# Performance work log

Hardware: AMD Instinct MI355X
Metric: run time of the kernel (lower is better)

## Reference

```python
import jax, jax.numpy as jnp
import numpy as np

N_GENOMES = 30000
N_GENES = 240000
N_SAMPLES = 128
N_SEQS = 80000


def setup_inputs() -> dict:
    key = jax.random.key(0)
    k0, k1, k2, k3, k4 = jax.random.split(key, 5)
    A = jax.random.normal(k0, (N_GENOMES, N_SAMPLES), dtype=jnp.float32)  # log-abundance
    B = jax.random.normal(k1, (N_GENOMES, N_SAMPLES), dtype=jnp.float32)  # log-PTR
    pos = jax.random.uniform(k2, (N_GENES,), dtype=jnp.float32)           # dist from ori, in [0,1)
    genome_idx = jnp.sort(jax.random.randint(k3, (N_GENES,), 0, N_GENOMES))  # block one-hot of `members`
    seq_idx = jax.random.randint(k4, (N_GENES,), 0, N_SEQS)               # gene -> md5 sequence map
    return {"A": A, "B": B, "pos": pos, "genome_idx": genome_idx, "seq_idx": seq_idx}


def reference(A, B, pos, genome_idx, seq_idx):
    # G = members @ A + 1 - dists @ B, where members/dists are one-hot per gene row
    # -> gather rows of A and B by genome assignment, scale B row by gene position.
    G = A[genome_idx] + 1.0 - pos[:, None] * B[genome_idx]   # (m, s)
    # gene_to_seq @ exp(G) -> segment sum of exp(G) over gene->sequence assignment
    return jax.ops.segment_sum(jnp.exp(G), seq_idx, num_segments=N_SEQS)  # (k, s)
```

## Files before the change

### kernel.cpp

```cpp
#include <hip/hip_runtime.h>
#include <hip/hip_fp16.h>

#define N_GENOMES 30000
#define N_GENES   240000
#define N_SAMPLES 128
#define N_SEQS    80000
#define CAP       32

#define SCATTER_BLOCKS  ((N_GENES + 255) / 256)
#define COMPRESS_BLOCKS ((N_GENOMES * 32) / 256)

typedef float        f32x4 __attribute__((ext_vector_type(4)));
typedef unsigned int u32x4 __attribute__((ext_vector_type(4)));

#define LOG2E 1.4426950408889634f

#if __has_builtin(__builtin_amdgcn_exp2f)
#define EXP2F(x) __builtin_amdgcn_exp2f(x)
#else
#define EXP2F(x) exp2f(x)
#endif

__global__ __launch_bounds__(256) void prep_kernel(
    const float* __restrict__ A,
    const float* __restrict__ B,
    const float* __restrict__ pos,
    const int*   __restrict__ genome_idx,
    const int*   __restrict__ seq_idx,
    int*          __restrict__ cnt,
    unsigned int* __restrict__ bucket,
    float4*       __restrict__ AB16)
{
    int b = blockIdx.x;
    if (b < SCATTER_BLOCKS) {
        int gene = b * 256 + threadIdx.x;
        if (gene >= N_GENES) return;
        int   s = seq_idx[gene];
        int   g = genome_idx[gene];
        float p = pos[gene];
        unsigned int q   = (unsigned int)(p * 131072.0f);
        unsigned int rec = (unsigned int)g | (q << 15);
        int slot = atomicAdd(&cnt[s], 1);
        if (slot < CAP) bucket[s * CAP + slot] = rec;
    } else {
        int idx = (b - SCATTER_BLOCKS) * 256 + threadIdx.x;
        f32x4 a  = __builtin_nontemporal_load((const f32x4*)A + idx);
        f32x4 bb = __builtin_nontemporal_load((const f32x4*)B + idx);
        __half2 h[4];
        h[0] = __floats2half2_rn((a.x + 1.0f) * LOG2E, (a.y + 1.0f) * LOG2E);
        h[1] = __floats2half2_rn((a.z + 1.0f) * LOG2E, (a.w + 1.0f) * LOG2E);
        h[2] = __floats2half2_rn(bb.x * LOG2E, bb.y * LOG2E);
        h[3] = __floats2half2_rn(bb.z * LOG2E, bb.w * LOG2E);
        AB16[idx] = *reinterpret_cast<float4*>(h);
    }
}

__global__ __launch_bounds__(256) void accum_kernel(
    const float4*       __restrict__ AB16,
    const int*          __restrict__ cnt,
    const unsigned int* __restrict__ bucket,
    float*              __restrict__ out)
{
    int idx  = blockIdx.x * blockDim.x + threadIdx.x;
    int seq  = idx >> 5;
    int quad = idx & 31;
    if (seq >= N_SEQS) return;

    const u32x4* bk4 = reinterpret_cast<const u32x4*>(bucket + seq * CAP);
    u32x4 r4 = bk4[0];
    int   n  = cnt[seq];
    if (n > CAP) n = CAP;

    float4 acc = make_float4(0.f, 0.f, 0.f, 0.f);

    {
        unsigned int r[4] = { r4.x, r4.y, r4.z, r4.w };
        float4 raw[4];
        #pragma unroll
        for (int j = 0; j < 4; ++j) {
            unsigned int g = (j < n) ? (r[j] & 0x7fffu) : 0u;
            raw[j] = AB16[g * 32 + quad];
        }
        #pragma unroll
        for (int j = 0; j < 4; ++j) {
            float p = (float)(r[j] >> 15) * (1.0f / 131072.0f);
            const __half2* hp = reinterpret_cast<const __half2*>(&raw[j]);
            float2 a01 = __half22float2(hp[0]);
            float2 a23 = __half22float2(hp[1]);
            float2 b01 = __half22float2(hp[2]);
            float2 b23 = __half22float2(hp[3]);
            if (j < n) {
                acc.x += EXP2F(a01.x - p * b01.x);
                acc.y += EXP2F(a01.y - p * b01.y);
                acc.z += EXP2F(a23.x - p * b23.x);
                acc.w += EXP2F(a23.y - p * b23.y);
            }
        }
    }

    if (n > 4) {
        for (int i0 = 4; i0 < n; i0 += 4) {
            u32x4 t4 = bk4[i0 >> 2];
            unsigned int r[4] = { t4.x, t4.y, t4.z, t4.w };
            float4 raw[4];
            #pragma unroll
            for (int j = 0; j < 4; ++j) {
                unsigned int g = (i0 + j < n) ? (r[j] & 0x7fffu) : 0u;
                raw[j] = AB16[g * 32 + quad];
            }
            #pragma unroll
            for (int j = 0; j < 4; ++j) {
                float p = (float)(r[j] >> 15) * (1.0f / 131072.0f);
                const __half2* hp = reinterpret_cast<const __half2*>(&raw[j]);
                float2 a01 = __half22float2(hp[0]);
                float2 a23 = __half22float2(hp[1]);
                float2 b01 = __half22float2(hp[2]);
                float2 b23 = __half22float2(hp[3]);
                if (i0 + j < n) {
                    acc.x += EXP2F(a01.x - p * b01.x);
                    acc.y += EXP2F(a01.y - p * b01.y);
                    acc.z += EXP2F(a23.x - p * b23.x);
                    acc.w += EXP2F(a23.y - p * b23.y);
                }
            }
        }
    }

    f32x4 o = { acc.x, acc.y, acc.z, acc.w };
    __builtin_nontemporal_store(o, (f32x4*)out + seq * 32 + quad);
}

extern "C" void kernel_launch(void* const* d_in, const int* in_sizes, int n_in,
                              void* d_out, int out_size, void* d_ws, size_t ws_size,
                              hipStream_t stream) {
    const float* A    = (const float*)d_in[0];
    const float* B    = (const float*)d_in[1];
    const float* pos  = (const float*)d_in[2];
    const int*   gidx = (const int*)d_in[3];
    const int*   sidx = (const int*)d_in[4];
    float*       out  = (float*)d_out;

    char*         ws     = (char*)d_ws;
    float4*       AB16   = (float4*)ws;
    int*          cnt    = (int*)(ws + (size_t)N_GENOMES * 32 * 16);
    unsigned int* bucket = (unsigned int*)(cnt + N_SEQS);

    hipMemsetAsync(cnt, 0, N_SEQS * sizeof(int), stream);

    prep_kernel<<<SCATTER_BLOCKS + COMPRESS_BLOCKS, 256, 0, stream>>>(
        A, B, pos, gidx, sidx, cnt, bucket, AB16);

    const int total = N_SEQS * 32;
    accum_kernel<<<total / 256, 256, 0, stream>>>(
        AB16, cnt, bucket, out);
}
```

Measured before the change: 125.1 us.

## Replace bucketed gather with per-gene atomic scatter into zeroed output

Drops the bucket-building prep pass, the fp16 compressed copy of A and B, and the per-sequence gather kernel. A single kernel now walks genes (each wave handles one gene row of 128 samples), computes exp in fp32 directly from A and B, and atomically adds into the output, which is zeroed with a memset first. Block-to-XCD mapping is arranged so each XCD handles a contiguous gene range, aiming for L2 locality on the sorted genome rows. This removes a kernel launch and the bucket CAP truncation, but costs a full 41 MB output memset plus about 30M float atomics to global memory, and the summation order is no longer deterministic.

```diff
diff --git a/kernel.cpp b/kernel.cpp
--- a/kernel.cpp
+++ b/kernel.cpp
@@ -1,17 +1,9 @@
 #include <hip/hip_runtime.h>
-#include <hip/hip_fp16.h>
 
 #define N_GENOMES 30000
 #define N_GENES   240000
 #define N_SAMPLES 128
 #define N_SEQS    80000
-#define CAP       32
-
-#define SCATTER_BLOCKS  ((N_GENES + 255) / 256)
-#define COMPRESS_BLOCKS ((N_GENOMES * 32) / 256)
-
-typedef float        f32x4 __attribute__((ext_vector_type(4)));
-typedef unsigned int u32x4 __attribute__((ext_vector_type(4)));
 
 #define LOG2E 1.4426950408889634f
 
@@ -21,113 +13,47 @@
 #define EXP2F(x) exp2f(x)
 #endif
 
-__global__ __launch_bounds__(256) void prep_kernel(
+#define GENES_PER_XCD (N_GENES / 8)
+#define BLOCKS_PER_XCD 256
+#define GENES_PER_BLOCK 118
+
+__global__ __launch_bounds__(256) void gene_kernel(
     const float* __restrict__ A,
     const float* __restrict__ B,
     const float* __restrict__ pos,
     const int*   __restrict__ genome_idx,
     const int*   __restrict__ seq_idx,
-    int*          __restrict__ cnt,
-    unsigned int* __restrict__ bucket,
-    float4*       __restrict__ AB16)
+    float*       __restrict__ out)
 {
-    int b = blockIdx.x;
-    if (b < SCATTER_BLOCKS) {
-        int gene = b * 256 + threadIdx.x;
-        if (gene >= N_GENES) return;
-        int   s = seq_idx[gene];
-        int   g = genome_idx[gene];
-        float p = pos[gene];
-        unsigned int q   = (unsigned int)(p * 131072.0f);
-        unsigned int rec = (unsigned int)g | (q << 15);
-        int slot = atomicAdd(&cnt[s], 1);
-        if (slot < CAP) bucket[s * CAP + slot] = rec;
-    } else {
-        int idx = (b - SCATTER_BLOCKS) * 256 + threadIdx.x;
-        f32x4 a  = __builtin_nontemporal_load((const f32x4*)A + idx);
-        f32x4 bb = __builtin_nontemporal_load((const f32x4*)B + idx);
-        __half2 h[4];
-        h[0] = __floats2half2_rn((a.x + 1.0f) * LOG2E, (a.y + 1.0f) * LOG2E);
-        h[1] = __floats2half2_rn((a.z + 1.0f) * LOG2E, (a.w + 1.0f) * LOG2E);
-        h[2] = __floats2half2_rn(bb.x * LOG2E, bb.y * LOG2E);
-        h[3] = __floats2half2_rn(bb.z * LOG2E, bb.w * LOG2E);
-        AB16[idx] = *reinterpret_cast<float4*>(h);
+    const int lane = threadIdx.x & 63;
+    const int wav  = threadIdx.x >> 6;
+    const int xcd  = blockIdx.x & 7;
+    const int jb   = blockIdx.x >> 3;
+
+    const int gbase = xcd * GENES_PER_XCD + jb * GENES_PER_BLOCK;
+    const int glim  = (xcd + 1) * GENES_PER_XCD;
+    int gend = gbase + GENES_PER_BLOCK;
+    if (gend > glim) gend = glim;
+
+    for (int g = gbase + wav; g < gend; g += 4) {
+        int   gm = genome_idx[g];
+        int   s  = seq_idx[g];
+        float pl = pos[g] * LOG2E;
+
+        const float2* Ar = (const float2*)(A + (size_t)gm * N_SAMPLES);
+        const float2* Br = (const float2*)(B + (size_t)gm * N_SAMPLES);
+        float2 a = Ar[lane];
+        float2 b = Br[lane];
+
+        float x0 = fmaf(b.x, -pl, fmaf(a.x, LOG2E, LOG2E));
+        float x1 = fmaf(b.y, -pl, fmaf(a.y, LOG2E, LOG2E));
+        float e0 = EXP2F(x0);
+        float e1 = EXP2F(x1);
+
+        float* o = out + (size_t)s * N_SAMPLES + lane * 2;
+        atomicAdd(o,     e0);
+        atomicAdd(o + 1, e1);
     }
-}
-
-__global__ __launch_bounds__(256) void accum_kernel(
-    const float4*       __restrict__ AB16,
-    const int*          __restrict__ cnt,
-    const unsigned int* __restrict__ bucket,
-    float*              __restrict__ out)
-{
-    int idx  = blockIdx.x * blockDim.x + threadIdx.x;
-    int seq  = idx >> 5;
-    int quad = idx & 31;
-    if (seq >= N_SEQS) return;
-
-    const u32x4* bk4 = reinterpret_cast<const u32x4*>(bucket + seq * CAP);
-    u32x4 r4 = bk4[0];
-    int   n  = cnt[seq];
-    if (n > CAP) n = CAP;
-
-    float4 acc = make_float4(0.f, 0.f, 0.f, 0.f);
-
-    {
-        unsigned int r[4] = { r4.x, r4.y, r4.z, r4.w };
-        float4 raw[4];
-        #pragma unroll
-        for (int j = 0; j < 4; ++j) {
-            unsigned int g = (j < n) ? (r[j] & 0x7fffu) : 0u;
-            raw[j] = AB16[g * 32 + quad];
-        }
-        #pragma unroll
-        for (int j = 0; j < 4; ++j) {
-            float p = (float)(r[j] >> 15) * (1.0f / 131072.0f);
-            const __half2* hp = reinterpret_cast<const __half2*>(&raw[j]);
-            float2 a01 = __half22float2(hp[0]);
-            float2 a23 = __half22float2(hp[1]);
-            float2 b01 = __half22float2(hp[2]);
-            float2 b23 = __half22float2(hp[3]);
-            if (j < n) {
-                acc.x += EXP2F(a01.x - p * b01.x);
-                acc.y += EXP2F(a01.y - p * b01.y);
-                acc.z += EXP2F(a23.x - p * b23.x);
-                acc.w += EXP2F(a23.y - p * b23.y);
-            }
-        }
-    }
-
-    if (n > 4) {
-        for (int i0 = 4; i0 < n; i0 += 4) {
-            u32x4 t4 = bk4[i0 >> 2];
-            unsigned int r[4] = { t4.x, t4.y, t4.z, t4.w };
-            float4 raw[4];
-            #pragma unroll
-            for (int j = 0; j < 4; ++j) {
-                unsigned int g = (i0 + j < n) ? (r[j] & 0x7fffu) : 0u;
-                raw[j] = AB16[g * 32 + quad];
-            }
-            #pragma unroll
-            for (int j = 0; j < 4; ++j) {
-                float p = (float)(r[j] >> 15) * (1.0f / 131072.0f);
-                const __half2* hp = reinterpret_cast<const __half2*>(&raw[j]);
-                float2 a01 = __half22float2(hp[0]);
-                float2 a23 = __half22float2(hp[1]);
-                float2 b01 = __half22float2(hp[2]);
-                float2 b23 = __half22float2(hp[3]);
-                if (i0 + j < n) {
-                    acc.x += EXP2F(a01.x - p * b01.x);
-                    acc.y += EXP2F(a01.y - p * b01.y);
-                    acc.z += EXP2F(a23.x - p * b23.x);
-                    acc.w += EXP2F(a23.y - p * b23.y);
-                }
-            }
-        }
-    }
-
-    f32x4 o = { acc.x, acc.y, acc.z, acc.w };
-    __builtin_nontemporal_store(o, (f32x4*)out + seq * 32 + quad);
 }
 
 extern "C" void kernel_launch(void* const* d_in, const int* in_sizes, int n_in,
@@ -140,17 +66,8 @@
     const int*   sidx = (const int*)d_in[4];
     float*       out  = (float*)d_out;
 
-    char*         ws     = (char*)d_ws;
-    float4*       AB16   = (float4*)ws;
-    int*          cnt    = (int*)(ws + (size_t)N_GENOMES * 32 * 16);
-    unsigned int* bucket = (unsigned int*)(cnt + N_SEQS);
+    hipMemsetAsync(out, 0, (size_t)N_SEQS * N_SAMPLES * sizeof(float), stream);
 
-    hipMemsetAsync(cnt, 0, N_SEQS * sizeof(int), stream);
-
-    prep_kernel<<<SCATTER_BLOCKS + COMPRESS_BLOCKS, 256, 0, stream>>>(
-        A, B, pos, gidx, sidx, cnt, bucket, AB16);
-
-    const int total = N_SEQS * 32;
-    accum_kernel<<<total / 256, 256, 0, stream>>>(
-        AB16, cnt, bucket, out);
+    gene_kernel<<<8 * BLOCKS_PER_XCD, 256, 0, stream>>>(
+        A, B, pos, gidx, sidx, out);
 }
```

After: 285.9 us. 2.28x slower.
